# Performance work log

Hardware: AMD Instinct MI355X
Metric: run time of the kernel (lower is better)

Reference implementation:

```python
import jax, jax.numpy as jnp
import numpy as np

N_NODES = 100000
N_EDGES = 1600000
IN_CH = 128
HID = 128
N_GRAPHS = 512


def setup_inputs() -> dict:
    key = jax.random.key(0)
    ks = jax.random.split(key, 16)
    x = jax.random.normal(ks[0], (N_NODES, IN_CH), dtype=jnp.float32)
    edge_index = jax.random.randint(ks[1], (2, N_EDGES), 0, N_NODES, dtype=jnp.int64)
    batch = jnp.sort(jax.random.randint(ks[2], (N_NODES,), 0, N_GRAPHS, dtype=jnp.int64))
    s = 1.0 / np.sqrt(HID)
    params = {
        'W1': jax.random.normal(ks[3], (IN_CH, HID), jnp.float32) / np.sqrt(IN_CH),
        'b1': jnp.zeros((HID,), jnp.float32),
        'W2': jax.random.normal(ks[4], (HID, HID), jnp.float32) * s,
        'b2': jnp.zeros((HID,), jnp.float32),
        'W3': jax.random.normal(ks[5], (HID, HID), jnp.float32) * s,
        'b3': jnp.zeros((HID,), jnp.float32),
        'Wf1': jax.random.normal(ks[6], (2 * HID, HID), jnp.float32) / np.sqrt(2 * HID),
        'bf1': jnp.zeros((HID,), jnp.float32),
        'Wf2': jax.random.normal(ks[7], (HID, HID // 2), jnp.float32) * s,
        'bf2': jnp.zeros((HID // 2,), jnp.float32),
        'Wf3': jax.random.normal(ks[8], (HID // 2, 1), jnp.float32) / np.sqrt(HID // 2),
        'bf3': jnp.zeros((1,), jnp.float32),
    }
    return {'x': x, 'edge_index': edge_index, 'batch': batch, 'n_graphs': N_GRAPHS, **params}


def _gcn_norm(edge_index, n_nodes):
    # add self-loops, then symmetric normalization D^{-1/2} (A+I) D^{-1/2}
    loops = jnp.arange(n_nodes, dtype=edge_index.dtype)
    src = jnp.concatenate([edge_index[0], loops])
    dst = jnp.concatenate([edge_index[1], loops])
    deg = jax.ops.segment_sum(jnp.ones_like(dst, dtype=jnp.float32), dst, num_segments=n_nodes)
    dinv = jnp.where(deg > 0, jax.lax.rsqrt(deg), 0.0)
    norm = dinv[src] * dinv[dst]  # [E + N]
    return src, dst, norm


def _gcn_conv(h, W, b, src, dst, norm, n_nodes):
    h = h @ W                                   # [N, H]
    msg = h[src] * norm[:, None]                # gather + edge scale
    agg = jax.ops.segment_sum(msg, dst, num_segments=n_nodes)  # scatter-add
    return agg + b


def reference(x, edge_index, batch, n_graphs, W1, b1, W2, b2, W3, b3, Wf1, bf1, Wf2, bf2, Wf3, bf3):
    n_nodes = x.shape[0]
    src, dst, norm = _gcn_norm(edge_index, n_nodes)

    h = jax.nn.relu(_gcn_conv(x, W1, b1, src, dst, norm, n_nodes))
    h_res = h
    h = jax.nn.relu(_gcn_conv(h, W2, b2, src, dst, norm, n_nodes)) + h_res
    h_res = h
    h = jax.nn.relu(_gcn_conv(h, W3, b3, src, dst, norm, n_nodes)) + h_res

    ones = jnp.ones((n_nodes, 1), jnp.float32)
    counts = jax.ops.segment_sum(ones, batch, num_segments=n_graphs)  # [G,1]
    g_mean = jax.ops.segment_sum(h, batch, num_segments=n_graphs) / jnp.maximum(counts, 1.0)
    g_max = jax.ops.segment_max(h, batch, num_segments=n_graphs)
    g = jnp.concatenate([g_mean, g_max], axis=1)  # [G, 2H]

    # MLP head (dropout is identity at inference)
    g = jax.nn.relu(g @ Wf1 + bf1)
    g = jax.nn.relu(g @ Wf2 + bf2)
    return g @ Wf3 + bf3  # [G, 1]
```

## Files before the change

### kernel.cpp

```cpp
#include <hip/hip_runtime.h>
#include <hip/hip_bf16.h>

#define NBMAX 128

typedef __attribute__((ext_vector_type(8))) short short8;
typedef __attribute__((ext_vector_type(4))) float f32x4;

__device__ inline unsigned short bf16_rne(float x) {
    unsigned u = __float_as_uint(x);
    u = (u + 0x7FFFu + ((u >> 16) & 1u)) >> 16;
    return (unsigned short)u;
}
__device__ inline float bf16_to_f(unsigned short h) {
    return __uint_as_float(((unsigned)h) << 16);
}
__device__ inline void split2(float v, short& h, short& lo) {
    unsigned short hb = bf16_rne(v);
    h = (short)hb;
    lo = (short)bf16_rne(v - bf16_to_f(hb));
}


__global__ __launch_bounds__(256) void k_bcnt(const int* __restrict__ dst, int E, int NB,
                                              int* __restrict__ bucket_cnt) {
    __shared__ int lcnt[NBMAX];
    int t = threadIdx.x;
    int base = blockIdx.x * 4096;
    for (int i = t; i < NB; i += 256) lcnt[i] = 0;
    __syncthreads();
#pragma unroll
    for (int i = 0; i < 16; i++) {
        int e = base + i * 256 + t;
        if (e < E) atomicAdd(&lcnt[dst[e] >> 10], 1);
    }
    __syncthreads();
    for (int i = t; i < NB; i += 256) {
        int c = lcnt[i];
        if (c) atomicAdd(&bucket_cnt[i], c);
    }
}

__global__ __launch_bounds__(128) void k_bscan(const int* __restrict__ bucket_cnt,
                                               int NB, int E, int N,
                                               int* __restrict__ bucket_off,
                                               int* __restrict__ bcur,
                                               int* __restrict__ rowstart) {
    __shared__ int sh[128];
    int t = threadIdx.x;
    int v = (t < NB) ? bucket_cnt[t] : 0;
    sh[t] = v;
    __syncthreads();
    for (int off = 1; off < 128; off <<= 1) {
        int x = (t >= off) ? sh[t - off] : 0;
        __syncthreads();
        sh[t] += x;
        __syncthreads();
    }
    if (t < NB) {
        int excl = sh[t] - v;
        bucket_off[t] = excl;
        bcur[t] = excl;
    }
    if (t == 0) {
        bucket_off[NB] = E;
        rowstart[N] = E;
    }
}

__global__ __launch_bounds__(256) void k_bucket(const int* __restrict__ src,
                                                const int* __restrict__ dst, int E, int NB,
                                                int* __restrict__ bcur,
                                                uint2* __restrict__ pairs) {
    __shared__ int lcnt[NBMAX];
    __shared__ int gbase[NBMAX];
    int t = threadIdx.x;
    int base = blockIdx.x * 4096;
    for (int i = t; i < NB; i += 256) lcnt[i] = 0;
    __syncthreads();
    int rank[16];
#pragma unroll
    for (int i = 0; i < 16; i++) {
        int e = base + i * 256 + t;
        rank[i] = (e < E) ? atomicAdd(&lcnt[dst[e] >> 10], 1) : -1;
    }
    __syncthreads();
    for (int i = t; i < NB; i += 256) {
        int c = lcnt[i];
        gbase[i] = c ? atomicAdd(&bcur[i], c) : 0;
    }
    __syncthreads();
#pragma unroll
    for (int i = 0; i < 16; i++) {
        int e = base + i * 256 + t;
        if (e < E) {
            int d = dst[e];
            pairs[gbase[d >> 10] + rank[i]] = make_uint2((unsigned)src[e], (unsigned)d);
        }
    }
}

__global__ __launch_bounds__(1024) void k_node(const uint2* __restrict__ pairs,
                                               const int* __restrict__ bucket_off, int N,
                                               int* __restrict__ rowstart,
                                               float* __restrict__ dinv,
                                               int* __restrict__ csr_src) {
    __shared__ int cnt_l[1024];
    __shared__ int cur_l[1024];
    __shared__ int wsum[16];
    int t = threadIdx.x;
    int lane = t & 63, wv = t >> 6;
    int b = blockIdx.x;
    int n0 = b << 10;
    int nn = min(1024, N - n0);
    cnt_l[t] = 0;
    __syncthreads();
    int e0 = bucket_off[b], e1 = bucket_off[b + 1];
    for (int e = e0 + t; e < e1; e += 1024) {
        atomicAdd(&cnt_l[(int)pairs[e].y - n0], 1);
    }
    __syncthreads();
    int c = cnt_l[t];
    int v = c;
#pragma unroll
    for (int off = 1; off < 64; off <<= 1) {
        int x = __shfl_up(v, off);
        if (lane >= off) v += x;
    }
    if (lane == 63) wsum[wv] = v;
    __syncthreads();
    if (wv == 0 && lane < 16) {
        int wval = wsum[lane];
#pragma unroll
        for (int off = 1; off < 16; off <<= 1) {
            int x = __shfl_up(wval, off);
            if (lane >= off) wval += x;
        }
        wsum[lane] = wval;
    }
    __syncthreads();
    int prefix = (wv > 0) ? wsum[wv - 1] : 0;
    int start = e0 + prefix + v - c;
    cur_l[t] = start;
    if (t < nn) {
        rowstart[n0 + t] = start;
        dinv[n0 + t] = rsqrtf((float)c + 1.0f);
    }
    __syncthreads();
    for (int e = e0 + t; e < e1; e += 1024) {
        uint2 p = pairs[e];
        int r = atomicAdd(&cur_l[(int)p.y - n0], 1);
        csr_src[r] = (int)p.x;
    }
}

__global__ __launch_bounds__(256) void k_wprep3(const float* __restrict__ W1,
                                                const float* __restrict__ W2,
                                                const float* __restrict__ W3,
                                                unsigned short* __restrict__ WH,
                                                unsigned short* __restrict__ WL,
                                                int* __restrict__ bucket_cnt) {
    if (blockIdx.x == 0 && threadIdx.x < NBMAX) bucket_cnt[threadIdx.x] = 0;
    int wi = blockIdx.x >> 6;
    int idx = (blockIdx.x & 63) * 256 + threadIdx.x;
    const float* W = (wi == 0) ? W1 : (wi == 1) ? W2 : W3;
    int j = idx & 7;
    int lane = (idx >> 3) & 63;
    int ct = (idx >> 9) & 7;
    int kc = idx >> 12;
    int k = kc * 32 + (lane >> 4) * 8 + j;
    int col = ct * 16 + (lane & 15);
    float v = W[k * 128 + col];
    unsigned short hb = bf16_rne(v);
    WH[wi * 16384 + idx] = hb;
    WL[wi * 16384 + idx] = bf16_rne(v - bf16_to_f(hb));
}


__global__ __launch_bounds__(256) void k_gemm3(const float* __restrict__ A,
                                               const unsigned short* __restrict__ WH,
                                               const unsigned short* __restrict__ WL,
                                               const float* __restrict__ dinv,
                                               unsigned short* __restrict__ U, int N) {
    int wv = threadIdx.x >> 6;
    int l = threadIdx.x & 63;
    int quad = l >> 4;
    int lm = l & 15;
    int rowBase = blockIdx.x * 128 + wv * 32;

    f32x4 acc[2][8] = {};

    int r0 = rowBase + lm;
    int r1 = rowBase + 16 + lm;

    for (int kc = 0; kc < 4; kc++) {
        int k0 = kc * 32 + quad * 8;
        float av0[8] = {}, av1[8] = {};
        if (r0 < N) {
            float4 a = *(const float4*)&A[(size_t)r0 * 128 + k0];
            float4 b = *(const float4*)&A[(size_t)r0 * 128 + k0 + 4];
            av0[0] = a.x; av0[1] = a.y; av0[2] = a.z; av0[3] = a.w;
            av0[4] = b.x; av0[5] = b.y; av0[6] = b.z; av0[7] = b.w;
        }
        if (r1 < N) {
            float4 a = *(const float4*)&A[(size_t)r1 * 128 + k0];
            float4 b = *(const float4*)&A[(size_t)r1 * 128 + k0 + 4];
            av1[0] = a.x; av1[1] = a.y; av1[2] = a.z; av1[3] = a.w;
            av1[4] = b.x; av1[5] = b.y; av1[6] = b.z; av1[7] = b.w;
        }
        short8 ah0, al0, ah1, al1;
#pragma unroll
        for (int j = 0; j < 8; j++) {
            short h, lo;
            split2(av0[j], h, lo); ah0[j] = h; al0[j] = lo;
            split2(av1[j], h, lo); ah1[j] = h; al1[j] = lo;
        }
#pragma unroll
        for (int ct = 0; ct < 8; ct++) {
            size_t fo = ((size_t)(kc * 8 + ct) * 64 + l) * 8;
            short8 wh = *(const short8*)&WH[fo];
            short8 wl = *(const short8*)&WL[fo];
            acc[0][ct] = __builtin_amdgcn_mfma_f32_16x16x32_bf16(ah0, wh, acc[0][ct], 0, 0, 0);
            acc[0][ct] = __builtin_amdgcn_mfma_f32_16x16x32_bf16(ah0, wl, acc[0][ct], 0, 0, 0);
            acc[0][ct] = __builtin_amdgcn_mfma_f32_16x16x32_bf16(al0, wh, acc[0][ct], 0, 0, 0);
            acc[1][ct] = __builtin_amdgcn_mfma_f32_16x16x32_bf16(ah1, wh, acc[1][ct], 0, 0, 0);
            acc[1][ct] = __builtin_amdgcn_mfma_f32_16x16x32_bf16(ah1, wl, acc[1][ct], 0, 0, 0);
            acc[1][ct] = __builtin_amdgcn_mfma_f32_16x16x32_bf16(al1, wh, acc[1][ct], 0, 0, 0);
        }
    }

#pragma unroll
    for (int rt = 0; rt < 2; rt++) {
#pragma unroll
        for (int reg = 0; reg < 4; reg++) {
            int row = rowBase + rt * 16 + quad * 4 + reg;
            if (row < N) {
                float dv = dinv[row];
#pragma unroll
                for (int ct = 0; ct < 8; ct++) {
                    U[(size_t)row * 128 + ct * 16 + lm] = bf16_rne(dv * acc[rt][ct][reg]);
                }
            }
        }
    }
}


template <int RES>
__global__ __launch_bounds__(256) void k_agg(const unsigned short* __restrict__ U,
                                             const int* __restrict__ rowstart,
                                             const int* __restrict__ csr_src,
                                             const float* __restrict__ dinv,
                                             const float* __restrict__ bias,
                                             float* __restrict__ H, int N) {
    int wave = threadIdx.x >> 6;
    int lane = threadIdx.x & 63;
    int n = blockIdx.x * 4 + wave;
    if (n >= N) return;
    int grp = lane >> 4;
    int li = lane & 15;
    int e0 = rowstart[n], e1 = rowstart[n + 1];
    int len = e1 - e0;
    int q0 = e0 + ((len * grp) >> 2);
    int q1 = e0 + ((len * (grp + 1)) >> 2);

    float a0 = 0.f, a1 = 0.f, a2 = 0.f, a3 = 0.f;
    float a4 = 0.f, a5 = 0.f, a6 = 0.f, a7 = 0.f;
    float b0 = 0.f, b1 = 0.f, b2 = 0.f, b3 = 0.f;
    float b4 = 0.f, b5 = 0.f, b6 = 0.f, b7 = 0.f;

    int e = q0;
    for (; e + 2 <= q1; e += 2) {
        int s0 = csr_src[e];
        int s1 = csr_src[e + 1];
        uint4 r0 = *(const uint4*)&U[(size_t)s0 * 128 + li * 8];
        uint4 r1 = *(const uint4*)&U[(size_t)s1 * 128 + li * 8];
        a0 += __uint_as_float(r0.x << 16);        a1 += __uint_as_float(r0.x & 0xFFFF0000u);
        a2 += __uint_as_float(r0.y << 16);        a3 += __uint_as_float(r0.y & 0xFFFF0000u);
        a4 += __uint_as_float(r0.z << 16);        a5 += __uint_as_float(r0.z & 0xFFFF0000u);
        a6 += __uint_as_float(r0.w << 16);        a7 += __uint_as_float(r0.w & 0xFFFF0000u);
        b0 += __uint_as_float(r1.x << 16);        b1 += __uint_as_float(r1.x & 0xFFFF0000u);
        b2 += __uint_as_float(r1.y << 16);        b3 += __uint_as_float(r1.y & 0xFFFF0000u);
        b4 += __uint_as_float(r1.z << 16);        b5 += __uint_as_float(r1.z & 0xFFFF0000u);
        b6 += __uint_as_float(r1.w << 16);        b7 += __uint_as_float(r1.w & 0xFFFF0000u);
    }
    if (e < q1) {
        int s0 = csr_src[e];
        uint4 r0 = *(const uint4*)&U[(size_t)s0 * 128 + li * 8];
        a0 += __uint_as_float(r0.x << 16);        a1 += __uint_as_float(r0.x & 0xFFFF0000u);
        a2 += __uint_as_float(r0.y << 16);        a3 += __uint_as_float(r0.y & 0xFFFF0000u);
        a4 += __uint_as_float(r0.z << 16);        a5 += __uint_as_float(r0.z & 0xFFFF0000u);
        a6 += __uint_as_float(r0.w << 16);        a7 += __uint_as_float(r0.w & 0xFFFF0000u);
    }
    a0 += b0; a1 += b1; a2 += b2; a3 += b3;
    a4 += b4; a5 += b5; a6 += b6; a7 += b7;

    a0 += __shfl_xor(a0, 16); a1 += __shfl_xor(a1, 16);
    a2 += __shfl_xor(a2, 16); a3 += __shfl_xor(a3, 16);
    a4 += __shfl_xor(a4, 16); a5 += __shfl_xor(a5, 16);
    a6 += __shfl_xor(a6, 16); a7 += __shfl_xor(a7, 16);
    a0 += __shfl_xor(a0, 32); a1 += __shfl_xor(a1, 32);
    a2 += __shfl_xor(a2, 32); a3 += __shfl_xor(a3, 32);
    a4 += __shfl_xor(a4, 32); a5 += __shfl_xor(a5, 32);
    a6 += __shfl_xor(a6, 32); a7 += __shfl_xor(a7, 32);

    if (grp == 0) {
        uint4 qs = *(const uint4*)&U[(size_t)n * 128 + li * 8];
        float4 bi0 = *(const float4*)&bias[li * 8];
        float4 bi1 = *(const float4*)&bias[li * 8 + 4];
        float dn = dinv[n];
        float4 o0, o1v;
        o0.x = fmaxf(dn * (a0 + __uint_as_float(qs.x << 16)) + bi0.x, 0.f);
        o0.y = fmaxf(dn * (a1 + __uint_as_float(qs.x & 0xFFFF0000u)) + bi0.y, 0.f);
        o0.z = fmaxf(dn * (a2 + __uint_as_float(qs.y << 16)) + bi0.z, 0.f);
        o0.w = fmaxf(dn * (a3 + __uint_as_float(qs.y & 0xFFFF0000u)) + bi0.w, 0.f);
        o1v.x = fmaxf(dn * (a4 + __uint_as_float(qs.z << 16)) + bi1.x, 0.f);
        o1v.y = fmaxf(dn * (a5 + __uint_as_float(qs.z & 0xFFFF0000u)) + bi1.y, 0.f);
        o1v.z = fmaxf(dn * (a6 + __uint_as_float(qs.w << 16)) + bi1.z, 0.f);
        o1v.w = fmaxf(dn * (a7 + __uint_as_float(qs.w & 0xFFFF0000u)) + bi1.w, 0.f);
        size_t hi = (size_t)n * 128 + li * 8;
        if (RES) {
            float4 h0 = *(const float4*)&H[hi];
            float4 h1 = *(const float4*)&H[hi + 4];
            o0.x += h0.x; o0.y += h0.y; o0.z += h0.z; o0.w += h0.w;
            o1v.x += h1.x; o1v.y += h1.y; o1v.z += h1.z; o1v.w += h1.w;
        }
        *(float4*)&H[hi] = o0;
        *(float4*)&H[hi + 4] = o1v;
    }
}


__global__ __launch_bounds__(256) void k_head(const float* __restrict__ H,
                                              const int* __restrict__ batch, int N, int G,
                                              const float* __restrict__ Wf1,
                                              const float* __restrict__ bf1,
                                              const float* __restrict__ Wf2,
                                              const float* __restrict__ bf2,
                                              const float* __restrict__ Wf3,
                                              const float* __restrict__ bf3,
                                              float* __restrict__ out) {
    __shared__ float ssum[256];
    __shared__ float smax[256];
    __shared__ float grow[256];
    __shared__ float o1[128];
    __shared__ float o2[64];
    int g = blockIdx.x;
    int t = threadIdx.x;
    int i0, i1;
    {
        int lo = 0, hi = N;
        while (lo < hi) { int m = (lo + hi) >> 1; if (batch[m] < g) lo = m + 1; else hi = m; }
        i0 = lo;
        lo = i0; hi = N;
        while (lo < hi) { int m = (lo + hi) >> 1; if (batch[m] < g + 1) lo = m + 1; else hi = m; }
        i1 = lo;
    }
    int c = t & 127;
    int half = t >> 7;
    int cn = i1 - i0;
    int mid = i0 + (cn >> 1);
    int a0 = half ? mid : i0;
    int a1 = half ? i1 : mid;
    float s = 0.f, m = -3.4e38f;
    for (int i = a0; i < a1; i++) {
        float v = H[(size_t)i * 128 + c];
        s += v;
        m = fmaxf(m, v);
    }
    ssum[t] = s;
    smax[t] = m;
    __syncthreads();
    if (half == 0) {
        float st = ssum[c] + ssum[c + 128];
        float mt = fmaxf(smax[c], smax[c + 128]);
        grow[c] = (cn > 0) ? st / (float)cn : 0.f;
        grow[128 + c] = (cn > 0) ? mt : 0.f;
    }
    __syncthreads();
    if (t < 128) {
        float acc = bf1[t];
#pragma unroll 8
        for (int k = 0; k < 256; k++) acc = fmaf(grow[k], Wf1[k * 128 + t], acc);
        o1[t] = fmaxf(acc, 0.f);
    }
    __syncthreads();
    if (t < 64) {
        float a2 = bf2[t];
#pragma unroll 8
        for (int k = 0; k < 128; k++) a2 = fmaf(o1[k], Wf2[k * 64 + t], a2);
        o2[t] = fmaxf(a2, 0.f);
    }
    __syncthreads();
    if (t < 64) {
        float p = o2[t] * Wf3[t];
        for (int off = 32; off > 0; off >>= 1) p += __shfl_down(p, off);
        if (t == 0) out[g] = p + bf3[0];
    }
}


extern "C" void kernel_launch(void* const* d_in, const int* in_sizes, int n_in,
                              void* d_out, int out_size, void* d_ws, size_t ws_size,
                              hipStream_t stream) {
    const float* x = (const float*)d_in[0];
    const int* ei = (const int*)d_in[1];
    const int* batch = (const int*)d_in[2];
    const float* W1 = (const float*)d_in[4];
    const float* b1 = (const float*)d_in[5];
    const float* W2 = (const float*)d_in[6];
    const float* b2 = (const float*)d_in[7];
    const float* W3 = (const float*)d_in[8];
    const float* b3 = (const float*)d_in[9];
    const float* Wf1 = (const float*)d_in[10];
    const float* bf1 = (const float*)d_in[11];
    const float* Wf2 = (const float*)d_in[12];
    const float* bf2 = (const float*)d_in[13];
    const float* Wf3 = (const float*)d_in[14];
    const float* bf3 = (const float*)d_in[15];

    const int N = in_sizes[0] / 128;
    const int E = in_sizes[1] / 2;
    const int G = out_size;

    const int* src = ei;
    const int* dst = ei + E;

    char* w = (char*)d_ws;
    size_t off = 0;
    auto alloc = [&](size_t bytes) -> void* {
        void* p = w + off;
        off += (bytes + 255) / 256 * 256;
        return p;
    };
    unsigned short* U = (unsigned short*)alloc((size_t)N * 128 * 2);
    float* H = (float*)alloc((size_t)N * 128 * 4);
    uint2* pairs = (uint2*)alloc((size_t)E * 8);
    int* csr_src = (int*)alloc((size_t)E * 4);
    int* rowstart = (int*)alloc((size_t)(N + 1) * 4);
    float* dinv = (float*)alloc((size_t)N * 4);
    int* bucket_cnt = (int*)alloc(NBMAX * 4);
    int* bucket_off = (int*)alloc((NBMAX + 1) * 4);
    int* bcur = (int*)alloc(NBMAX * 4);
    unsigned short* WH = (unsigned short*)alloc(3 * 16384 * 2);
    unsigned short* WL = (unsigned short*)alloc(3 * 16384 * 2);
    float* out = (float*)d_out;

    const int NB = (N + 1023) >> 10;
    const int ebk = (E + 4095) / 4096;

    k_wprep3<<<dim3(192), dim3(256), 0, stream>>>(W1, W2, W3, WH, WL, bucket_cnt);

    k_bcnt<<<dim3(ebk), dim3(256), 0, stream>>>(dst, E, NB, bucket_cnt);
    k_bscan<<<dim3(1), dim3(128), 0, stream>>>(bucket_cnt, NB, E, N, bucket_off, bcur, rowstart);
    k_bucket<<<dim3(ebk), dim3(256), 0, stream>>>(src, dst, E, NB, bcur, pairs);
    k_node<<<dim3(NB), dim3(1024), 0, stream>>>(pairs, bucket_off, N, rowstart, dinv, csr_src);

    const int gemmGrid = (N + 127) / 128;
    const int aggGrid = (N + 3) / 4;

    k_gemm3<<<dim3(gemmGrid), dim3(256), 0, stream>>>(x, WH, WL, dinv, U, N);
    k_agg<0><<<dim3(aggGrid), dim3(256), 0, stream>>>(U, rowstart, csr_src, dinv, b1, H, N);
    k_gemm3<<<dim3(gemmGrid), dim3(256), 0, stream>>>(H, WH + 16384, WL + 16384, dinv, U, N);
    k_agg<1><<<dim3(aggGrid), dim3(256), 0, stream>>>(U, rowstart, csr_src, dinv, b2, H, N);
    k_gemm3<<<dim3(gemmGrid), dim3(256), 0, stream>>>(H, WH + 32768, WL + 32768, dinv, U, N);
    k_agg<1><<<dim3(aggGrid), dim3(256), 0, stream>>>(U, rowstart, csr_src, dinv, b3, H, N);

    k_head<<<dim3(G), dim3(256), 0, stream>>>(H, batch, N, G, Wf1, bf1, Wf2, bf2, Wf3, bf3, out);
}
```

Measured before the change: 510.5 us.

## Pack bucket pairs into 32-bit words and stage GEMM tiles through LDS

Bucketed edge pairs are packed into a single 32-bit word (local dst index in the high bits, src in the low 17 bits) instead of a uint2. This halves the traffic of the bucket write and the two node-kernel reads. The GEMM now loads A tiles coalesced into shared memory and stages the bf16 output tile in LDS so the global stores are coalesced 8-byte writes. The packing assumes source ids fit in 17 bits, which holds for 100k nodes but fails for larger graphs. The GEMM also adds block-level synchronisation.

New measurement: 527.7 us. 3.4% more time.

```diff
diff --git a/kernel.cpp b/kernel.cpp
--- a/kernel.cpp
+++ b/kernel.cpp
@@ -70,7 +70,7 @@
 __global__ __launch_bounds__(256) void k_bucket(const int* __restrict__ src,
                                                 const int* __restrict__ dst, int E, int NB,
                                                 int* __restrict__ bcur,
-                                                uint2* __restrict__ pairs) {
+                                                unsigned* __restrict__ pairs) {
     __shared__ int lcnt[NBMAX];
     __shared__ int gbase[NBMAX];
     int t = threadIdx.x;
@@ -94,12 +94,13 @@
         int e = base + i * 256 + t;
         if (e < E) {
             int d = dst[e];
-            pairs[gbase[d >> 10] + rank[i]] = make_uint2((unsigned)src[e], (unsigned)d);
-        }
-    }
-}
-
-__global__ __launch_bounds__(1024) void k_node(const uint2* __restrict__ pairs,
+            pairs[gbase[d >> 10] + rank[i]] =
+                ((unsigned)(d & 1023) << 17) | (unsigned)src[e];
+        }
+    }
+}
+
+__global__ __launch_bounds__(1024) void k_node(const unsigned* __restrict__ pairs,
                                                const int* __restrict__ bucket_off, int N,
                                                int* __restrict__ rowstart,
                                                float* __restrict__ dinv,
@@ -116,7 +117,7 @@
     __syncthreads();
     int e0 = bucket_off[b], e1 = bucket_off[b + 1];
     for (int e = e0 + t; e < e1; e += 1024) {
-        atomicAdd(&cnt_l[(int)pairs[e].y - n0], 1);
+        atomicAdd(&cnt_l[pairs[e] >> 17], 1);
     }
     __syncthreads();
     int c = cnt_l[t];
@@ -147,9 +148,9 @@
     }
     __syncthreads();
     for (int e = e0 + t; e < e1; e += 1024) {
-        uint2 p = pairs[e];
-        int r = atomicAdd(&cur_l[(int)p.y - n0], 1);
-        csr_src[r] = (int)p.x;
+        unsigned p = pairs[e];
+        int r = atomicAdd(&cur_l[p >> 17], 1);
+        csr_src[r] = (int)(p & 0x1FFFFu);
     }
 }
 
@@ -181,31 +182,50 @@
                                                const unsigned short* __restrict__ WL,
                                                const float* __restrict__ dinv,
                                                unsigned short* __restrict__ U, int N) {
-    int wv = threadIdx.x >> 6;
-    int l = threadIdx.x & 63;
+    __shared__ __align__(16) char smem[128 * 132 * 2];
+    float (*Ash)[34] = (float(*)[34])smem;
+    unsigned short (*Ust)[132] = (unsigned short(*)[132])smem;
+
+    int t = threadIdx.x;
+    int wv = t >> 6;
+    int l = t & 63;
     int quad = l >> 4;
     int lm = l & 15;
-    int rowBase = blockIdx.x * 128 + wv * 32;
+    int rowBase = blockIdx.x * 128;
 
     f32x4 acc[2][8] = {};
 
-    int r0 = rowBase + lm;
-    int r1 = rowBase + 16 + lm;
-
     for (int kc = 0; kc < 4; kc++) {
-        int k0 = kc * 32 + quad * 8;
-        float av0[8] = {}, av1[8] = {};
-        if (r0 < N) {
-            float4 a = *(const float4*)&A[(size_t)r0 * 128 + k0];
-            float4 b = *(const float4*)&A[(size_t)r0 * 128 + k0 + 4];
-            av0[0] = a.x; av0[1] = a.y; av0[2] = a.z; av0[3] = a.w;
-            av0[4] = b.x; av0[5] = b.y; av0[6] = b.z; av0[7] = b.w;
-        }
-        if (r1 < N) {
-            float4 a = *(const float4*)&A[(size_t)r1 * 128 + k0];
-            float4 b = *(const float4*)&A[(size_t)r1 * 128 + k0 + 4];
-            av1[0] = a.x; av1[1] = a.y; av1[2] = a.z; av1[3] = a.w;
-            av1[4] = b.x; av1[5] = b.y; av1[6] = b.z; av1[7] = b.w;
+        float4 v[4];
+#pragma unroll
+        for (int i = 0; i < 4; i++) {
+            int idx = t + i * 256;
+            int row = idx >> 3;
+            int c4 = idx & 7;
+            int gr = rowBase + row;
+            v[i] = make_float4(0.f, 0.f, 0.f, 0.f);
+            if (gr < N) v[i] = *(const float4*)&A[(size_t)gr * 128 + kc * 32 + c4 * 4];
+        }
+        __syncthreads();
+#pragma unroll
+        for (int i = 0; i < 4; i++) {
+            int idx = t + i * 256;
+            int row = idx >> 3;
+            int c4 = idx & 7;
+            *(float2*)&Ash[row][c4 * 4] = make_float2(v[i].x, v[i].y);
+            *(float2*)&Ash[row][c4 * 4 + 2] = make_float2(v[i].z, v[i].w);
+        }
+        __syncthreads();
+
+        int lr0 = wv * 32 + lm;
+        int lr1 = wv * 32 + 16 + lm;
+        float av0[8], av1[8];
+#pragma unroll
+        for (int jj = 0; jj < 4; jj++) {
+            float2 p0 = *(const float2*)&Ash[lr0][quad * 8 + jj * 2];
+            float2 p1 = *(const float2*)&Ash[lr1][quad * 8 + jj * 2];
+            av0[jj * 2] = p0.x; av0[jj * 2 + 1] = p0.y;
+            av1[jj * 2] = p1.x; av1[jj * 2 + 1] = p1.y;
         }
         short8 ah0, al0, ah1, al1;
 #pragma unroll
@@ -228,18 +248,30 @@
         }
     }
 
+    __syncthreads();
 #pragma unroll
     for (int rt = 0; rt < 2; rt++) {
 #pragma unroll
         for (int reg = 0; reg < 4; reg++) {
-            int row = rowBase + rt * 16 + quad * 4 + reg;
-            if (row < N) {
-                float dv = dinv[row];
-#pragma unroll
-                for (int ct = 0; ct < 8; ct++) {
-                    U[(size_t)row * 128 + ct * 16 + lm] = bf16_rne(dv * acc[rt][ct][reg]);
-                }
+            int lrow = wv * 32 + rt * 16 + quad * 4 + reg;
+            int grow_ = rowBase + lrow;
+            float dv = (grow_ < N) ? dinv[grow_] : 0.f;
+#pragma unroll
+            for (int ct = 0; ct < 8; ct++) {
+                Ust[lrow][ct * 16 + lm] = bf16_rne(dv * acc[rt][ct][reg]);
             }
+        }
+    }
+    __syncthreads();
+#pragma unroll
+    for (int i = 0; i < 16; i++) {
+        int idx = t + i * 256;
+        int row = idx >> 5;
+        int c = idx & 31;
+        int gr = rowBase + row;
+        if (gr < N) {
+            uint2 vv = *(const uint2*)&Ust[row][c * 4];
+            *(uint2*)&U[(size_t)gr * 128 + c * 4] = vv;
         }
     }
 }
@@ -434,7 +466,7 @@
     };
     unsigned short* U = (unsigned short*)alloc((size_t)N * 128 * 2);
     float* H = (float*)alloc((size_t)N * 128 * 4);
-    uint2* pairs = (uint2*)alloc((size_t)E * 8);
+    unsigned* pairs = (unsigned*)alloc((size_t)E * 4);
     int* csr_src = (int*)alloc((size_t)E * 4);
     int* rowstart = (int*)alloc((size_t)(N + 1) * 4);
     float* dinv = (float*)alloc((size_t)N * 4);
```

## Compact CSR build: 32-bit packed pairs, LDS-staged bucket scatter, smaller buckets

Applied to the files above, without the earlier changes.

Reworks the CSR construction. Buckets shrink to 512 nodes, and each (src, local dst) pair is packed into one 32-bit word, which halves the traffic on the intermediate pairs buffer. k_bucket now sorts its chunk by bucket in LDS before writing, so global writes are contiguous per bucket instead of scattered. k_node stages csr_src in LDS and writes it out coalesced. This adds LDS use and extra syncs, and the 17-bit src packing assumes N < 131072.

Result: faster. 496.4 us (-2.8%).

```diff
diff --git a/kernel.cpp b/kernel.cpp
--- a/kernel.cpp
+++ b/kernel.cpp
@@ -1,7 +1,11 @@
 #include <hip/hip_runtime.h>
 #include <hip/hip_bf16.h>
 
-#define NBMAX 128
+#define NBMAX 256
+#define BSH 9
+#define BMSK 511
+#define CHUNK 4096
+#define NCAP 10240
 
 typedef __attribute__((ext_vector_type(8))) short short8;
 typedef __attribute__((ext_vector_type(4))) float f32x4;
@@ -25,13 +29,13 @@
                                               int* __restrict__ bucket_cnt) {
     __shared__ int lcnt[NBMAX];
     int t = threadIdx.x;
-    int base = blockIdx.x * 4096;
+    int base = blockIdx.x * CHUNK;
     for (int i = t; i < NB; i += 256) lcnt[i] = 0;
     __syncthreads();
 #pragma unroll
     for (int i = 0; i < 16; i++) {
         int e = base + i * 256 + t;
-        if (e < E) atomicAdd(&lcnt[dst[e] >> 10], 1);
+        if (e < E) atomicAdd(&lcnt[dst[e] >> BSH], 1);
     }
     __syncthreads();
     for (int i = t; i < NB; i += 256) {
@@ -40,17 +44,17 @@
     }
 }
 
-__global__ __launch_bounds__(128) void k_bscan(const int* __restrict__ bucket_cnt,
+__global__ __launch_bounds__(256) void k_bscan(const int* __restrict__ bucket_cnt,
                                                int NB, int E, int N,
                                                int* __restrict__ bucket_off,
                                                int* __restrict__ bcur,
                                                int* __restrict__ rowstart) {
-    __shared__ int sh[128];
+    __shared__ int sh[NBMAX];
     int t = threadIdx.x;
     int v = (t < NB) ? bucket_cnt[t] : 0;
     sh[t] = v;
     __syncthreads();
-    for (int off = 1; off < 128; off <<= 1) {
+    for (int off = 1; off < NBMAX; off <<= 1) {
         int x = (t >= off) ? sh[t - off] : 0;
         __syncthreads();
         sh[t] += x;
@@ -70,53 +74,81 @@
 __global__ __launch_bounds__(256) void k_bucket(const int* __restrict__ src,
                                                 const int* __restrict__ dst, int E, int NB,
                                                 int* __restrict__ bcur,
-                                                uint2* __restrict__ pairs) {
+                                                unsigned* __restrict__ pairs) {
     __shared__ int lcnt[NBMAX];
+    __shared__ int loff[NBMAX];
     __shared__ int gbase[NBMAX];
+    __shared__ unsigned plds[CHUNK];
+    __shared__ unsigned char blds[CHUNK];
     int t = threadIdx.x;
-    int base = blockIdx.x * 4096;
-    for (int i = t; i < NB; i += 256) lcnt[i] = 0;
-    __syncthreads();
-    int rank[16];
-#pragma unroll
-    for (int i = 0; i < 16; i++) {
-        int e = base + i * 256 + t;
-        rank[i] = (e < E) ? atomicAdd(&lcnt[dst[e] >> 10], 1) : -1;
-    }
-    __syncthreads();
-    for (int i = t; i < NB; i += 256) {
-        int c = lcnt[i];
-        gbase[i] = c ? atomicAdd(&bcur[i], c) : 0;
-    }
-    __syncthreads();
+    int base = blockIdx.x * CHUNK;
+    for (int i = t; i < NBMAX; i += 256) lcnt[i] = 0;
+    __syncthreads();
+    int rank[16], bid[16];
+    unsigned pk[16];
 #pragma unroll
     for (int i = 0; i < 16; i++) {
         int e = base + i * 256 + t;
         if (e < E) {
             int d = dst[e];
-            pairs[gbase[d >> 10] + rank[i]] = make_uint2((unsigned)src[e], (unsigned)d);
-        }
-    }
-}
-
-__global__ __launch_bounds__(1024) void k_node(const uint2* __restrict__ pairs,
-                                               const int* __restrict__ bucket_off, int N,
-                                               int* __restrict__ rowstart,
-                                               float* __restrict__ dinv,
-                                               int* __restrict__ csr_src) {
-    __shared__ int cnt_l[1024];
-    __shared__ int cur_l[1024];
-    __shared__ int wsum[16];
+            int b = d >> BSH;
+            bid[i] = b;
+            pk[i] = ((unsigned)(d & BMSK) << 17) | (unsigned)src[e];
+            rank[i] = atomicAdd(&lcnt[b], 1);
+        } else bid[i] = -1;
+    }
+    __syncthreads();
+    loff[t] = lcnt[t];
+    __syncthreads();
+    for (int off = 1; off < NBMAX; off <<= 1) {
+        int x = (t >= off) ? loff[t - off] : 0;
+        __syncthreads();
+        loff[t] += x;
+        __syncthreads();
+    }
+    if (t < NB) {
+        int c = lcnt[t];
+        gbase[t] = c ? atomicAdd(&bcur[t], c) : 0;
+    }
+    __syncthreads();
+#pragma unroll
+    for (int i = 0; i < 16; i++) {
+        int b = bid[i];
+        if (b >= 0) {
+            int pos = loff[b] - lcnt[b] + rank[i];
+            plds[pos] = pk[i];
+            blds[pos] = (unsigned char)b;
+        }
+    }
+    __syncthreads();
+    int total = min(E - base, CHUNK);
+    for (int i = t; i < total; i += 256) {
+        int b = blds[i];
+        int local = i - (loff[b] - lcnt[b]);
+        pairs[gbase[b] + local] = plds[i];
+    }
+}
+
+__global__ __launch_bounds__(512) void k_node(const unsigned* __restrict__ pairs,
+                                              const int* __restrict__ bucket_off, int N,
+                                              int* __restrict__ rowstart,
+                                              float* __restrict__ dinv,
+                                              int* __restrict__ csr_src) {
+    __shared__ int cnt_l[512];
+    __shared__ int cur_l[512];
+    __shared__ int wsum[8];
+    __shared__ int stage[NCAP];
     int t = threadIdx.x;
     int lane = t & 63, wv = t >> 6;
     int b = blockIdx.x;
-    int n0 = b << 10;
-    int nn = min(1024, N - n0);
+    int n0 = b << BSH;
+    int nn = min(512, N - n0);
     cnt_l[t] = 0;
     __syncthreads();
     int e0 = bucket_off[b], e1 = bucket_off[b + 1];
-    for (int e = e0 + t; e < e1; e += 1024) {
-        atomicAdd(&cnt_l[(int)pairs[e].y - n0], 1);
+    int len = e1 - e0;
+    for (int e = e0 + t; e < e1; e += 512) {
+        atomicAdd(&cnt_l[pairs[e] >> 17], 1);
     }
     __syncthreads();
     int c = cnt_l[t];
@@ -128,28 +160,40 @@
     }
     if (lane == 63) wsum[wv] = v;
     __syncthreads();
-    if (wv == 0 && lane < 16) {
-        int wval = wsum[lane];
-#pragma unroll
-        for (int off = 1; off < 16; off <<= 1) {
+    if (t < 8) {
+        int wval = wsum[t];
+#pragma unroll
+        for (int off = 1; off < 8; off <<= 1) {
             int x = __shfl_up(wval, off);
             if (lane >= off) wval += x;
         }
-        wsum[lane] = wval;
+        wsum[t] = wval;
     }
     __syncthreads();
     int prefix = (wv > 0) ? wsum[wv - 1] : 0;
     int start = e0 + prefix + v - c;
-    cur_l[t] = start;
     if (t < nn) {
         rowstart[n0 + t] = start;
         dinv[n0 + t] = rsqrtf((float)c + 1.0f);
     }
-    __syncthreads();
-    for (int e = e0 + t; e < e1; e += 1024) {
-        uint2 p = pairs[e];
-        int r = atomicAdd(&cur_l[(int)p.y - n0], 1);
-        csr_src[r] = (int)p.x;
+    if (len <= NCAP) {
+        cur_l[t] = start - e0;
+        __syncthreads();
+        for (int e = e0 + t; e < e1; e += 512) {
+            unsigned p = pairs[e];
+            int r = atomicAdd(&cur_l[p >> 17], 1);
+            stage[r] = (int)(p & 0x1FFFFu);
+        }
+        __syncthreads();
+        for (int i = t; i < len; i += 512) csr_src[e0 + i] = stage[i];
+    } else {
+        cur_l[t] = start;
+        __syncthreads();
+        for (int e = e0 + t; e < e1; e += 512) {
+            unsigned p = pairs[e];
+            int r = atomicAdd(&cur_l[p >> 17], 1);
+            csr_src[r] = (int)(p & 0x1FFFFu);
+        }
     }
 }
 
@@ -434,7 +478,7 @@
     };
     unsigned short* U = (unsigned short*)alloc((size_t)N * 128 * 2);
     float* H = (float*)alloc((size_t)N * 128 * 4);
-    uint2* pairs = (uint2*)alloc((size_t)E * 8);
+    unsigned* pairs = (unsigned*)alloc((size_t)E * 4);
     int* csr_src = (int*)alloc((size_t)E * 4);
     int* rowstart = (int*)alloc((size_t)(N + 1) * 4);
     float* dinv = (float*)alloc((size_t)N * 4);
@@ -445,15 +489,15 @@
     unsigned short* WL = (unsigned short*)alloc(3 * 16384 * 2);
     float* out = (float*)d_out;
 
-    const int NB = (N + 1023) >> 10;
-    const int ebk = (E + 4095) / 4096;
+    const int NB = (N + BMSK) >> BSH;
+    const int ebk = (E + CHUNK - 1) / CHUNK;
 
     k_wprep3<<<dim3(192), dim3(256), 0, stream>>>(W1, W2, W3, WH, WL, bucket_cnt);
 
     k_bcnt<<<dim3(ebk), dim3(256), 0, stream>>>(dst, E, NB, bucket_cnt);
-    k_bscan<<<dim3(1), dim3(128), 0, stream>>>(bucket_cnt, NB, E, N, bucket_off, bcur, rowstart);
+    k_bscan<<<dim3(1), dim3(NBMAX), 0, stream>>>(bucket_cnt, NB, E, N, bucket_off, bcur, rowstart);
     k_bucket<<<dim3(ebk), dim3(256), 0, stream>>>(src, dst, E, NB, bcur, pairs);
-    k_node<<<dim3(NB), dim3(1024), 0, stream>>>(pairs, bucket_off, N, rowstart, dinv, csr_src);
+    k_node<<<dim3(NB), dim3(512), 0, stream>>>(pairs, bucket_off, N, rowstart, dinv, csr_src);
 
     const int gemmGrid = (N + 127) / 128;
     const int aggGrid = (N + 3) / 4;
```
